# Kernel tuning notes

Measured on AMD Instinct MI355X. Metric: run time of the kernel, lower is better.

The kernel has to match this reference:

```python
import jax, jax.numpy as jnp
import numpy as np

N = 8192
IN_F = 512
OUT_F = 512
ALPHA = 0.2          # LeakyReLU negative slope
NEG_INF = -9e15      # matches masked_fill value in the torch source


def setup_inputs() -> dict:
    key = jax.random.key(0)
    k1, k2, k3, k4, k5 = jax.random.split(key, 5)
    x = jax.random.normal(k1, (N, IN_F), dtype=jnp.float32)
    adj = jax.random.randint(k2, (N, N), 0, 2, dtype=jnp.int32)
    # nn.Linear(in, out, bias=False) stores weight as [out, in]
    W = jax.random.normal(k3, (OUT_F, IN_F), dtype=jnp.float32) / np.sqrt(IN_F)
    # nn.Linear(2*out, 1) weight [1, 2*out] split into the two halves that
    # act on h_i (a1) and h_j (a2): a([h_i, h_j]) = a1.h_i + a2.h_j
    a1 = jax.random.normal(k4, (OUT_F,), dtype=jnp.float32) / np.sqrt(2 * OUT_F)
    a2 = jax.random.normal(k5, (OUT_F,), dtype=jnp.float32) / np.sqrt(2 * OUT_F)
    return {"x": x, "adj": adj, "W": W, "a1": a1, "a2": a2}


def reference(x, adj, W, a1, a2):
    # h = W(x)                                  [N, OUT_F]
    h = x @ W.T
    # e[i, j] = leakyrelu(a . [h_i, h_j]) = leakyrelu(a1.h_i + a2.h_j)
    # (identical math to the N^2 concat in the source, without materializing it)
    src = h @ a1                                # [N]
    dst = h @ a2                                # [N]
    e = jax.nn.leaky_relu(src[:, None] + dst[None, :], negative_slope=ALPHA)
    e = jnp.where(adj == 0, jnp.float32(NEG_INF), e)
    attention = jax.nn.softmax(e, axis=1)       # [N, N]
    # dropout prob is 0.0 (eval-equivalent), so it is the identity
    h_prime = attention @ h                     # [N, OUT_F]
    return h_prime
```

## Files before the change

### kernel.cpp

```cpp
#include <hip/hip_runtime.h>
#include <hip/hip_bf16.h>
#include <stdint.h>

#define NN 8192
#define KF 512
#define ALPHA 0.2f
#define NTT 64

typedef __bf16 bf16;
typedef __bf16 bf16x4 __attribute__((ext_vector_type(4)));
typedef __bf16 bf16x8 __attribute__((ext_vector_type(8)));
typedef float  f32x4  __attribute__((ext_vector_type(4)));
typedef float  f32x16 __attribute__((ext_vector_type(16)));

static constexpr size_t OFF_HQ  = 0;
static constexpr size_t OFF_XB  = (size_t)8 << 20;
static constexpr size_t OFF_WB  = (size_t)16 << 20;
static constexpr size_t OFF_SRC = OFF_WB + ((size_t)512 << 10);
static constexpr size_t OFF_DST = OFF_SRC + (size_t)NN * 4;
static constexpr size_t OFF_PRT = (size_t)17 << 20;
static constexpr size_t OFF_PDN = OFF_PRT + ((size_t)32 << 20);


__global__ void k_cvt(const float* __restrict__ x, const float* __restrict__ W,
                      bf16* __restrict__ xb, bf16* __restrict__ wb) {
    const int XQ = (NN * KF) / 4;
    const int TQ = XQ + (KF * KF) / 4;
    for (int i = blockIdx.x * blockDim.x + threadIdx.x; i < TQ;
         i += gridDim.x * blockDim.x) {
        const float4* s;
        bf16* d;
        int o;
        if (i < XQ) { s = (const float4*)x; d = xb; o = i; }
        else        { s = (const float4*)W; d = wb; o = i - XQ; }
        float4 v = s[o];
        bf16x4 b;
        b[0] = (bf16)v.x; b[1] = (bf16)v.y; b[2] = (bf16)v.z; b[3] = (bf16)v.w;
        *(bf16x4*)(d + (size_t)o * 4) = b;
    }
}

__global__ __launch_bounds__(256) void k_gemm(
    const bf16* __restrict__ xb, const bf16* __restrict__ wb,
    bf16* __restrict__ hQ, float* __restrict__ srcv, float* __restrict__ dstv,
    const float* __restrict__ a1, const float* __restrict__ a2) {
    const int tid = threadIdx.x;
    const int wv = tid >> 6;
    const int l = tid & 63;
    const int task = blockIdx.x * 4 + wv;
    const int rg = task >> 3, cc = task & 7;
    const int i0 = rg * 16, c0 = cc * 64;
    const int lr16 = l & 15, lk = l >> 4;

    f32x4 acc0 = {0.f,0.f,0.f,0.f}, acc1 = acc0, acc2 = acc0, acc3 = acc0;

    const bf16* ap  = xb + (size_t)(i0 + lr16) * KF + lk * 8;
    const bf16* bp0 = wb + (size_t)(c0 +  0 + lr16) * KF + lk * 8;
    const bf16* bp1 = wb + (size_t)(c0 + 16 + lr16) * KF + lk * 8;
    const bf16* bp2 = wb + (size_t)(c0 + 32 + lr16) * KF + lk * 8;
    const bf16* bp3 = wb + (size_t)(c0 + 48 + lr16) * KF + lk * 8;

#pragma unroll 4
    for (int k = 0; k < 16; ++k) {
        bf16x8 a  = *(const bf16x8*)(ap  + k * 32);
        bf16x8 b0 = *(const bf16x8*)(bp0 + k * 32);
        bf16x8 b1 = *(const bf16x8*)(bp1 + k * 32);
        bf16x8 b2 = *(const bf16x8*)(bp2 + k * 32);
        bf16x8 b3 = *(const bf16x8*)(bp3 + k * 32);
        acc0 = __builtin_amdgcn_mfma_f32_16x16x32_bf16(a, b0, acc0, 0, 0, 0);
        acc1 = __builtin_amdgcn_mfma_f32_16x16x32_bf16(a, b1, acc1, 0, 0, 0);
        acc2 = __builtin_amdgcn_mfma_f32_16x16x32_bf16(a, b2, acc2, 0, 0, 0);
        acc3 = __builtin_amdgcn_mfma_f32_16x16x32_bf16(a, b3, acc3, 0, 0, 0);
    }

    const int ib = i0 + lk * 4;
    const int jt = ib >> 6, kq = (ib >> 3) & 7, jr0 = ib & 7;
    float sr[4] = {0.f,0.f,0.f,0.f}, dr[4] = {0.f,0.f,0.f,0.f};
#pragma unroll
    for (int ct = 0; ct < 4; ++ct) {
        const f32x4 av = (ct == 0) ? acc0 : (ct == 1) ? acc1 : (ct == 2) ? acc2 : acc3;
        const int c = c0 + ct * 16 + lr16;
        const float A1 = a1[c], A2 = a2[c];
        bf16x4 hb;
#pragma unroll
        for (int r = 0; r < 4; ++r) {
            float h = av[r];
            sr[r] += h * A1;
            dr[r] += h * A2;
            hb[r] = (bf16)h;
        }
        *(bf16x4*)(hQ + ((size_t)(jt * 8 + kq) * 512 + c) * 8 + jr0) = hb;
    }
#pragma unroll
    for (int r = 0; r < 4; ++r) {
        float s = sr[r], d = dr[r];
        s += __shfl_xor(s, 1, 64); d += __shfl_xor(d, 1, 64);
        s += __shfl_xor(s, 2, 64); d += __shfl_xor(d, 2, 64);
        s += __shfl_xor(s, 4, 64); d += __shfl_xor(d, 4, 64);
        s += __shfl_xor(s, 8, 64); d += __shfl_xor(d, 8, 64);
        if (lr16 == 0) {
            atomicAdd(srcv + ib + r, s);
            atomicAdd(dstv + ib + r, d);
        }
    }
}

__global__ __launch_bounds__(512) void k_attn(
    const int* __restrict__ adj, const bf16* __restrict__ hQ,
    const float* __restrict__ srcv, const float* __restrict__ dstv,
    float* __restrict__ part, float* __restrict__ pden) {
    __shared__ bf16 pl[2][64][72];

    const int tid = threadIdx.x;
    const int l = tid & 63;
    const int wv = tid >> 6;
    const int bid = blockIdx.x;
    const int xg = bid & 7, qg = bid >> 3;
    const int js = xg >> 2;
    const int rt = qg * 4 + (xg & 3);
    const int i0 = rt * 64;
    const int jbase = js * 4096;

    const int pr = tid >> 3;
    const int pj = (tid & 7) * 8;
    const float si = srcv[i0 + pr];

    const int lhi = l >> 5;
    const int l31 = l & 31;
    const int cA = wv * 64 + l31;

    const int*   adjp = adj  + (size_t)(i0 + pr) * NN + jbase + pj;
    const float* dstp = dstv + jbase + pj;
    const bf16*  hqb  = hQ + (size_t)cA * 8;
    const size_t tq0  = (size_t)js * 512;

    f32x16 acc00 = {0.f}, acc01 = {0.f}, acc10 = {0.f}, acc11 = {0.f};
    float dacc = 0.f;

    int4   aC0 = *(const int4*)(adjp);
    int4   aC1 = *(const int4*)(adjp + 4);
    float4 dC0 = *(const float4*)(dstp);
    float4 dC1 = *(const float4*)(dstp + 4);
    bf16x8 bf[8];
#pragma unroll
    for (int k2 = 0; k2 < 4; ++k2) {
        bf[k2 * 2]     = *(const bf16x8*)(hqb + (tq0 + k2 * 2 + lhi) * 4096);
        bf[k2 * 2 + 1] = *(const bf16x8*)(hqb + (tq0 + k2 * 2 + lhi) * 4096 + 256);
    }

    for (int t = 0; t < NTT; ++t) {
        float w0, w1, w2, w3, w4, w5, w6, w7, e;
        e = si + dC0.x; e = fmaxf(e, ALPHA * e); w0 = aC0.x ? __expf(e) : 0.f;
        e = si + dC0.y; e = fmaxf(e, ALPHA * e); w1 = aC0.y ? __expf(e) : 0.f;
        e = si + dC0.z; e = fmaxf(e, ALPHA * e); w2 = aC0.z ? __expf(e) : 0.f;
        e = si + dC0.w; e = fmaxf(e, ALPHA * e); w3 = aC0.w ? __expf(e) : 0.f;
        e = si + dC1.x; e = fmaxf(e, ALPHA * e); w4 = aC1.x ? __expf(e) : 0.f;
        e = si + dC1.y; e = fmaxf(e, ALPHA * e); w5 = aC1.y ? __expf(e) : 0.f;
        e = si + dC1.z; e = fmaxf(e, ALPHA * e); w6 = aC1.z ? __expf(e) : 0.f;
        e = si + dC1.w; e = fmaxf(e, ALPHA * e); w7 = aC1.w ? __expf(e) : 0.f;
        bf16x8 pb;
        pb[0] = (bf16)w0; pb[1] = (bf16)w1; pb[2] = (bf16)w2; pb[3] = (bf16)w3;
        pb[4] = (bf16)w4; pb[5] = (bf16)w5; pb[6] = (bf16)w6; pb[7] = (bf16)w7;
        *(bf16x8*)(&pl[t & 1][pr][pj]) = pb;
        dacc += ((w0 + w1) + (w2 + w3)) + ((w4 + w5) + (w6 + w7));

        bf16x8 bn[8];
        if (t + 1 < NTT) {
            aC0 = *(const int4*)(adjp + (t + 1) * 64);
            aC1 = *(const int4*)(adjp + (t + 1) * 64 + 4);
            dC0 = *(const float4*)(dstp + (t + 1) * 64);
            dC1 = *(const float4*)(dstp + (t + 1) * 64 + 4);
            const size_t tqn = tq0 + (size_t)(t + 1) * 8;
#pragma unroll
            for (int k2 = 0; k2 < 4; ++k2) {
                bn[k2 * 2]     = *(const bf16x8*)(hqb + (tqn + k2 * 2 + lhi) * 4096);
                bn[k2 * 2 + 1] = *(const bf16x8*)(hqb + (tqn + k2 * 2 + lhi) * 4096 + 256);
            }
        }

        asm volatile("s_waitcnt lgkmcnt(0)" ::: "memory");
        __builtin_amdgcn_s_barrier();

        const bf16* plc = &pl[t & 1][0][0];
#pragma unroll
        for (int k = 0; k < 4; ++k) {
            const int ko = k * 16 + lhi * 8;
            bf16x8 a0  = *(const bf16x8*)(plc + l31 * 72 + ko);
            bf16x8 a1f = *(const bf16x8*)(plc + (32 + l31) * 72 + ko);
            acc00 = __builtin_amdgcn_mfma_f32_32x32x16_bf16(a0,  bf[k*2],   acc00, 0,0,0);
            acc01 = __builtin_amdgcn_mfma_f32_32x32x16_bf16(a0,  bf[k*2+1], acc01, 0,0,0);
            acc10 = __builtin_amdgcn_mfma_f32_32x32x16_bf16(a1f, bf[k*2],   acc10, 0,0,0);
            acc11 = __builtin_amdgcn_mfma_f32_32x32x16_bf16(a1f, bf[k*2+1], acc11, 0,0,0);
        }
        if (t + 1 < NTT) {
#pragma unroll
            for (int q = 0; q < 8; ++q) bf[q] = bn[q];
        }
    }

    float* pp = part + (size_t)js * NN * KF;
#pragma unroll
    for (int g = 0; g < 16; ++g) {
        const int row = (g & 3) + 8 * (g >> 2) + 4 * lhi;
        pp[(size_t)(i0 + row) * KF + cA]           = acc00[g];
        pp[(size_t)(i0 + row) * KF + cA + 32]      = acc01[g];
        pp[(size_t)(i0 + 32 + row) * KF + cA]      = acc10[g];
        pp[(size_t)(i0 + 32 + row) * KF + cA + 32] = acc11[g];
    }
    dacc += __shfl_xor(dacc, 1, 64);
    dacc += __shfl_xor(dacc, 2, 64);
    dacc += __shfl_xor(dacc, 4, 64);
    if ((tid & 7) == 0) pden[(size_t)js * NN + i0 + pr] = dacc;
}

__global__ void k_red(const float* __restrict__ part, const float* __restrict__ pden,
                      float* __restrict__ out) {
    int idx = blockIdx.x * blockDim.x + threadIdx.x;
    const float4 p0 = *(const float4*)(part + (size_t)idx * 4);
    const float4 p1 = *(const float4*)(part + (size_t)NN * KF + (size_t)idx * 4);
    int i = idx >> 7;
    float inv = 1.f / (pden[i] + pden[NN + i]);
    float4 o;
    o.x = (p0.x + p1.x) * inv;
    o.y = (p0.y + p1.y) * inv;
    o.z = (p0.z + p1.z) * inv;
    o.w = (p0.w + p1.w) * inv;
    *(float4*)(out + (size_t)idx * 4) = o;
}

extern "C" void kernel_launch(void* const* d_in, const int* in_sizes, int n_in,
                              void* d_out, int out_size, void* d_ws, size_t ws_size,
                              hipStream_t stream) {
    (void)in_sizes; (void)n_in; (void)out_size; (void)ws_size;
    const float* x  = (const float*)d_in[0];
    const int* adj  = (const int*)d_in[1];
    const float* W  = (const float*)d_in[2];
    const float* a1 = (const float*)d_in[3];
    const float* a2 = (const float*)d_in[4];
    float* out = (float*)d_out;
    char* ws = (char*)d_ws;

    bf16* hQ  = (bf16*)(ws + OFF_HQ);
    bf16* xb  = (bf16*)(ws + OFF_XB);
    bf16* wb  = (bf16*)(ws + OFF_WB);
    float* sv = (float*)(ws + OFF_SRC);
    float* dv = (float*)(ws + OFF_DST);
    float* part = (float*)(ws + OFF_PRT);
    float* pden = (float*)(ws + OFF_PDN);

    hipMemsetAsync(sv, 0, (size_t)2 * NN * sizeof(float), stream);
    k_cvt<<<2048, 256, 0, stream>>>(x, W, xb, wb);
    k_gemm<<<1024, 256, 0, stream>>>(xb, wb, hQ, sv, dv, a1, a2);
    k_attn<<<256, 512, 0, stream>>>(adj, hQ, sv, dv, part, pden);
    k_red<<<4096, 256, 0, stream>>>(part, pden, out);
}
```

Baseline: 472.3 us.

## Double attention block threads and prefetch adjacency two tiles ahead

The attention kernel now launches 1024 threads per block instead of 512. Each wave covers 32 output columns with two accumulators instead of 64 columns with four, and each thread computes 4 attention weights per tile instead of 8. Adjacency, dst and hQ loads are now double-buffered two tiles ahead in alternating A/B register sets, with the loop manually unrolled by two. The aim is more waves per CU to hide memory latency on the adjacency stream, at the cost of fewer MFMAs per LDS read and tighter register limits per thread.

```diff
diff --git a/kernel.cpp b/kernel.cpp
--- a/kernel.cpp
+++ b/kernel.cpp
@@ -105,7 +105,7 @@
     }
 }
 
-__global__ __launch_bounds__(512) void k_attn(
+__global__ __launch_bounds__(1024) void k_attn(
     const int* __restrict__ adj, const bf16* __restrict__ hQ,
     const float* __restrict__ srcv, const float* __restrict__ dstv,
     float* __restrict__ part, float* __restrict__ pden) {
@@ -121,96 +121,84 @@
     const int i0 = rt * 64;
     const int jbase = js * 4096;
 
-    const int pr = tid >> 3;
-    const int pj = (tid & 7) * 8;
+    const int pr = tid >> 4;
+    const int pj = (tid & 15) * 4;
     const float si = srcv[i0 + pr];
 
     const int lhi = l >> 5;
     const int l31 = l & 31;
-    const int cA = wv * 64 + l31;
+    const int cA = wv * 32 + l31;
 
     const int*   adjp = adj  + (size_t)(i0 + pr) * NN + jbase + pj;
     const float* dstp = dstv + jbase + pj;
     const bf16*  hqb  = hQ + (size_t)cA * 8;
     const size_t tq0  = (size_t)js * 512;
 
-    f32x16 acc00 = {0.f}, acc01 = {0.f}, acc10 = {0.f}, acc11 = {0.f};
+    f32x16 acc0 = {0.f}, acc1 = {0.f};
     float dacc = 0.f;
 
-    int4   aC0 = *(const int4*)(adjp);
-    int4   aC1 = *(const int4*)(adjp + 4);
-    float4 dC0 = *(const float4*)(dstp);
-    float4 dC1 = *(const float4*)(dstp + 4);
-    bf16x8 bf[8];
-#pragma unroll
-    for (int k2 = 0; k2 < 4; ++k2) {
-        bf[k2 * 2]     = *(const bf16x8*)(hqb + (tq0 + k2 * 2 + lhi) * 4096);
-        bf[k2 * 2 + 1] = *(const bf16x8*)(hqb + (tq0 + k2 * 2 + lhi) * 4096 + 256);
-    }
-
-    for (int t = 0; t < NTT; ++t) {
-        float w0, w1, w2, w3, w4, w5, w6, w7, e;
-        e = si + dC0.x; e = fmaxf(e, ALPHA * e); w0 = aC0.x ? __expf(e) : 0.f;
-        e = si + dC0.y; e = fmaxf(e, ALPHA * e); w1 = aC0.y ? __expf(e) : 0.f;
-        e = si + dC0.z; e = fmaxf(e, ALPHA * e); w2 = aC0.z ? __expf(e) : 0.f;
-        e = si + dC0.w; e = fmaxf(e, ALPHA * e); w3 = aC0.w ? __expf(e) : 0.f;
-        e = si + dC1.x; e = fmaxf(e, ALPHA * e); w4 = aC1.x ? __expf(e) : 0.f;
-        e = si + dC1.y; e = fmaxf(e, ALPHA * e); w5 = aC1.y ? __expf(e) : 0.f;
-        e = si + dC1.z; e = fmaxf(e, ALPHA * e); w6 = aC1.z ? __expf(e) : 0.f;
-        e = si + dC1.w; e = fmaxf(e, ALPHA * e); w7 = aC1.w ? __expf(e) : 0.f;
-        bf16x8 pb;
-        pb[0] = (bf16)w0; pb[1] = (bf16)w1; pb[2] = (bf16)w2; pb[3] = (bf16)w3;
-        pb[4] = (bf16)w4; pb[5] = (bf16)w5; pb[6] = (bf16)w6; pb[7] = (bf16)w7;
-        *(bf16x8*)(&pl[t & 1][pr][pj]) = pb;
-        dacc += ((w0 + w1) + (w2 + w3)) + ((w4 + w5) + (w6 + w7));
-
-        bf16x8 bn[8];
-        if (t + 1 < NTT) {
-            aC0 = *(const int4*)(adjp + (t + 1) * 64);
-            aC1 = *(const int4*)(adjp + (t + 1) * 64 + 4);
-            dC0 = *(const float4*)(dstp + (t + 1) * 64);
-            dC1 = *(const float4*)(dstp + (t + 1) * 64 + 4);
-            const size_t tqn = tq0 + (size_t)(t + 1) * 8;
-#pragma unroll
-            for (int k2 = 0; k2 < 4; ++k2) {
-                bn[k2 * 2]     = *(const bf16x8*)(hqb + (tqn + k2 * 2 + lhi) * 4096);
-                bn[k2 * 2 + 1] = *(const bf16x8*)(hqb + (tqn + k2 * 2 + lhi) * 4096 + 256);
-            }
-        }
-
-        asm volatile("s_waitcnt lgkmcnt(0)" ::: "memory");
-        __builtin_amdgcn_s_barrier();
-
-        const bf16* plc = &pl[t & 1][0][0];
-#pragma unroll
-        for (int k = 0; k < 4; ++k) {
-            const int ko = k * 16 + lhi * 8;
-            bf16x8 a0  = *(const bf16x8*)(plc + l31 * 72 + ko);
-            bf16x8 a1f = *(const bf16x8*)(plc + (32 + l31) * 72 + ko);
-            acc00 = __builtin_amdgcn_mfma_f32_32x32x16_bf16(a0,  bf[k*2],   acc00, 0,0,0);
-            acc01 = __builtin_amdgcn_mfma_f32_32x32x16_bf16(a0,  bf[k*2+1], acc01, 0,0,0);
-            acc10 = __builtin_amdgcn_mfma_f32_32x32x16_bf16(a1f, bf[k*2],   acc10, 0,0,0);
-            acc11 = __builtin_amdgcn_mfma_f32_32x32x16_bf16(a1f, bf[k*2+1], acc11, 0,0,0);
-        }
-        if (t + 1 < NTT) {
-#pragma unroll
-            for (int q = 0; q < 8; ++q) bf[q] = bn[q];
-        }
-    }
+    int4   ajA = *(const int4*)(adjp);
+    float4 dsA = *(const float4*)(dstp);
+    int4   ajB = *(const int4*)(adjp + 64);
+    float4 dsB = *(const float4*)(dstp + 64);
+    bf16x8 bfA[4], bfB[4];
+#pragma unroll
+    for (int k = 0; k < 4; ++k) {
+        bfA[k] = *(const bf16x8*)(hqb + (tq0 + k * 2 + lhi) * 4096);
+        bfB[k] = *(const bf16x8*)(hqb + (tq0 + 8 + k * 2 + lhi) * 4096);
+    }
+
+#define PHASE(T, AJ, DS, BF)                                                     \
+    {                                                                            \
+        const int t_ = (T);                                                      \
+        float w0, w1, w2, w3, e;                                                 \
+        e = si + DS.x; e = fmaxf(e, ALPHA * e); w0 = AJ.x ? __expf(e) : 0.f;     \
+        e = si + DS.y; e = fmaxf(e, ALPHA * e); w1 = AJ.y ? __expf(e) : 0.f;     \
+        e = si + DS.z; e = fmaxf(e, ALPHA * e); w2 = AJ.z ? __expf(e) : 0.f;     \
+        e = si + DS.w; e = fmaxf(e, ALPHA * e); w3 = AJ.w ? __expf(e) : 0.f;     \
+        bf16x4 pb;                                                               \
+        pb[0] = (bf16)w0; pb[1] = (bf16)w1; pb[2] = (bf16)w2; pb[3] = (bf16)w3;  \
+        *(bf16x4*)(&pl[t_ & 1][pr][pj]) = pb;                                    \
+        dacc += (w0 + w1) + (w2 + w3);                                           \
+        const int tp_ = (t_ + 2 < NTT) ? t_ + 2 : t_;    \
+        AJ = *(const int4*)(adjp + tp_ * 64);                                    \
+        DS = *(const float4*)(dstp + tp_ * 64);                                  \
+        asm volatile("s_waitcnt lgkmcnt(0)" ::: "memory");   \
+        __builtin_amdgcn_s_barrier();                                            \
+        const bf16* plc = &pl[t_ & 1][0][0];                                     \
+        _Pragma("unroll")                                                        \
+        for (int k = 0; k < 4; ++k) {                                            \
+            const int ko = k * 16 + lhi * 8;                                     \
+            bf16x8 a0  = *(const bf16x8*)(plc + l31 * 72 + ko);                  \
+            bf16x8 a1f = *(const bf16x8*)(plc + (32 + l31) * 72 + ko);           \
+            acc0 = __builtin_amdgcn_mfma_f32_32x32x16_bf16(a0,  BF[k], acc0, 0, 0, 0); \
+            acc1 = __builtin_amdgcn_mfma_f32_32x32x16_bf16(a1f, BF[k], acc1, 0, 0, 0); \
+        }                                                                        \
+        const size_t tqp_ = tq0 + (size_t)tp_ * 8;                               \
+        _Pragma("unroll")                                                        \
+        for (int k = 0; k < 4; ++k)                                              \
+            BF[k] = *(const bf16x8*)(hqb + (tqp_ + k * 2 + lhi) * 4096);         \
+    }
+
+#pragma unroll 1
+    for (int tt = 0; tt < NTT / 2; ++tt) {
+        PHASE(2 * tt,     ajA, dsA, bfA)
+        PHASE(2 * tt + 1, ajB, dsB, bfB)
+    }
+#undef PHASE
 
     float* pp = part + (size_t)js * NN * KF;
 #pragma unroll
     for (int g = 0; g < 16; ++g) {
         const int row = (g & 3) + 8 * (g >> 2) + 4 * lhi;
-        pp[(size_t)(i0 + row) * KF + cA]           = acc00[g];
-        pp[(size_t)(i0 + row) * KF + cA + 32]      = acc01[g];
-        pp[(size_t)(i0 + 32 + row) * KF + cA]      = acc10[g];
-        pp[(size_t)(i0 + 32 + row) * KF + cA + 32] = acc11[g];
+        pp[(size_t)(i0 + row) * KF + cA]      = acc0[g];
+        pp[(size_t)(i0 + 32 + row) * KF + cA] = acc1[g];
     }
     dacc += __shfl_xor(dacc, 1, 64);
     dacc += __shfl_xor(dacc, 2, 64);
     dacc += __shfl_xor(dacc, 4, 64);
-    if ((tid & 7) == 0) pden[(size_t)js * NN + i0 + pr] = dacc;
+    dacc += __shfl_xor(dacc, 8, 64);
+    if ((tid & 15) == 0) pden[(size_t)js * NN + i0 + pr] = dacc;
 }
 
 __global__ void k_red(const float* __restrict__ part, const float* __restrict__ pden,
@@ -251,6 +239,6 @@
     hipMemsetAsync(sv, 0, (size_t)2 * NN * sizeof(float), stream);
     k_cvt<<<2048, 256, 0, stream>>>(x, W, xb, wb);
     k_gemm<<<1024, 256, 0, stream>>>(xb, wb, hQ, sv, dv, a1, a2);
-    k_attn<<<256, 512, 0, stream>>>(adj, hQ, sv, dv, part, pden);
+    k_attn<<<256, 1024, 0, stream>>>(adj, hQ, sv, dv, part, pden);
     k_red<<<4096, 256, 0, stream>>>(part, pden, out);
 }
```

Measured after the change: 485.6 us. +2.8%, slower.
